# Kernel optimization log

Hardware: AMD Instinct MI355X
Metric: run time of the kernel (lower is better)

The kernel has to match this reference:

```python
import jax, jax.numpy as jnp
import numpy as np

HEADS = 8
DPH = 32  # n_features_per_head = 256 / 8
SCALE = 16.0  # sqrt(256)
EPS = 1e-5


def conv1x1(x, w, b):
    # x [B,C,H,W], w [O,C], b [O]
    return jnp.einsum('bchw,oc->bohw', x, w) + b[None, :, None, None]


def avg_pool2(x):
    # F.interpolate(scale_factor=0.5, bilinear, align_corners=False) with half-pixel
    # centers and integer-2 downsample is exactly 2x2 mean pooling.
    B, C, H, W = x.shape
    return x.reshape(B, C, H // 2, 2, W // 2, 2).mean(axis=(3, 5))


def grid_sample_bilinear(img, grid):
    # img [B,C,H,W], grid [B,Hg,Wg,2] (x,y) in [-1,1]; align_corners=False, zeros padding
    B, C, H, W = img.shape
    ix = (grid[..., 0] + 1.0) * (W * 0.5) - 0.5
    iy = (grid[..., 1] + 1.0) * (H * 0.5) - 0.5
    x0f = jnp.floor(ix); y0f = jnp.floor(iy)
    wx = ix - x0f; wy = iy - y0f
    x0 = x0f.astype(jnp.int32); y0 = y0f.astype(jnp.int32)
    flat = img.reshape(B, C, H * W)
    Hg, Wg = grid.shape[1], grid.shape[2]

    def gather(yy, xx):
        valid = ((xx >= 0) & (xx < W) & (yy >= 0) & (yy < H)).astype(img.dtype)
        idx = (jnp.clip(yy, 0, H - 1) * W + jnp.clip(xx, 0, W - 1)).reshape(B, 1, Hg * Wg)
        v = jnp.take_along_axis(flat, idx, axis=2).reshape(B, C, Hg, Wg)
        return v * valid[:, None]

    out = (gather(y0, x0) * ((1 - wy) * (1 - wx))[:, None]
           + gather(y0, x0 + 1) * ((1 - wy) * wx)[:, None]
           + gather(y0 + 1, x0) * (wy * (1 - wx))[:, None]
           + gather(y0 + 1, x0 + 1) * (wy * wx)[:, None])
    return out


def layernorm_channels(x, g, b):
    # LayerNormProxy(dim=1): normalize over channel axis per (b,h,w)
    mu = x.mean(axis=1, keepdims=True)
    var = ((x - mu) ** 2).mean(axis=1, keepdims=True)
    return (x - mu) / jnp.sqrt(var + EPS) * g[None, :, None, None] + b[None, :, None, None]


def setup_inputs() -> dict:
    key = jax.random.key(0)
    ks = jax.random.split(key, 16)
    B, D, H, W = 4, 256, 56, 56
    nH, nW = H // 2, W // 2
    s = 0.02
    inp = {
        'query': jax.random.normal(ks[0], (B, D, H, W), jnp.float32),
        'x': jax.random.normal(ks[1], (B, D, H, W), jnp.float32),
        'reference_points': jax.random.uniform(ks[2], (B * HEADS, nH, nW, 2), jnp.float32, -1.0, 1.0),
        'positional_embeddings': jax.random.normal(ks[3], (B, D, H, W), jnp.float32),
        'so_w1': jax.random.normal(ks[4], (D, 2 * D, 5, 5), jnp.float32) * s,
        'so_b1': jnp.zeros((D,), jnp.float32),
        'ln_g': jnp.ones((D,), jnp.float32),
        'ln_b': jnp.zeros((D,), jnp.float32),
        'so_w2': jax.random.normal(ks[5], (2 * HEADS, D), jnp.float32) * s,
        'so_b2': jax.random.normal(ks[6], (2 * HEADS,), jnp.float32),
        'q_w': jax.random.normal(ks[7], (D, D), jnp.float32) * s,
        'q_b': jnp.zeros((D,), jnp.float32),
        'k_w': jax.random.normal(ks[8], (DPH, DPH), jnp.float32) * s,
        'k_b': jnp.zeros((DPH,), jnp.float32),
        'v_w': jax.random.normal(ks[9], (DPH, DPH), jnp.float32) * s,
        'v_b': jnp.zeros((DPH,), jnp.float32),
        'o_w': jax.random.normal(ks[10], (D, D), jnp.float32) * s,
        'o_b': jnp.zeros((D,), jnp.float32),
    }
    return inp


def _forward(query, x, reference_points, positional_embeddings,
             so_w1, so_b1, ln_g, ln_b, so_w2, so_b2,
             q_w, q_b, k_w, k_b, v_w, v_b, o_w, o_b):
    B, D, H, W = query.shape
    # downsample + concat -> offset network
    rec = jnp.concatenate([avg_pool2(query), avg_pool2(x)], axis=1)  # [B,2D,nH,nW]
    h = jax.lax.conv_general_dilated(rec, so_w1, (1, 1), ((2, 2), (2, 2)),
                                     dimension_numbers=('NCHW', 'OIHW', 'NCHW'))
    h = h + so_b1[None, :, None, None]
    h = layernorm_channels(h, ln_g, ln_b)
    h = jax.nn.gelu(h, approximate=False)
    off = jnp.tanh(conv1x1(h, so_w2, so_b2))  # [B, 2*heads, nH, nW]
    nH, nW = off.shape[2], off.shape[3]
    # permute(0,2,3,1) -> view(B,nH,nW,heads,2) -> permute(0,3,1,2,4)
    off = off.transpose(0, 2, 3, 1).reshape(B, nH, nW, HEADS, 2)
    off = off.transpose(0, 3, 1, 2, 4).reshape(B * HEADS, nH, nW, 2)
    loc = jnp.clip(reference_points + off, -1.0, 1.0)
    sampled = grid_sample_bilinear(x.reshape(B * HEADS, DPH, H, W), loc)  # [B*h,dph,nH,nW]
    qe = query + positional_embeddings
    q = conv1x1(qe, q_w, q_b).reshape(B * HEADS, DPH, H * W)
    k = conv1x1(sampled, k_w, k_b).reshape(B * HEADS, DPH, nH * nW)
    v = conv1x1(sampled, v_w, v_b).reshape(B * HEADS, DPH, nH * nW)
    attn = jax.nn.softmax(jnp.einsum('bdq,bdk->bqk', q, k) / SCALE, axis=2)
    out = jnp.einsum('bqk,bdk->bdq', attn, v).reshape(B, D, H, W)
    return conv1x1(out, o_w, o_b)


def reference(query, x, reference_points, positional_embeddings,
              so_w1, so_b1, ln_g, ln_b, so_w2, so_b2,
              q_w, q_b, k_w, k_b, v_w, v_b, o_w, o_b):
    return _forward(query, x, reference_points, positional_embeddings,
                    so_w1, so_b1, ln_g, ln_b, so_w2, so_b2,
                    q_w, q_b, k_w, k_b, v_w, v_b, o_w, o_b)
```

## Files before the change

### kernel.cpp

```cpp
#include <hip/hip_runtime.h>
#include <hip/hip_bf16.h>

#define B_    4
#define D_    256
#define H_    56
#define W_    56
#define NH_   28
#define NW_   28
#define HEADS 8
#define DPH   32
#define NPOS  784
#define NS    3136
#define NSB   196

typedef unsigned short ushort_t;
typedef unsigned int uint_t;
typedef __attribute__((ext_vector_type(8))) short bf16x8;
typedef __attribute__((ext_vector_type(4))) float f32x4;

#define OFF_REC     0u
#define OFF_HPART   1605632u
#define OFF_WREPC   4816896u
#define OFF_LOC     8093696u
#define OFF_KTB     8946688u
#define OFF_VTB     9348096u
#define OFF_W256    9749568u
#define OFF_QPE     4816896u
#define OFF_QBF     0u
#define OFF_ATTNT   1605632u

__device__ __forceinline__ ushort_t bf16rne(float f) {
    uint_t u = __float_as_uint(f);
    return (ushort_t)((u + 0x7FFFu + ((u >> 16) & 1u)) >> 16);
}
__device__ __forceinline__ float ubf(ushort_t h) {
    return __uint_as_float(((uint_t)h) << 16);
}
__device__ __forceinline__ uint_t packsplit(float v) {
    ushort_t hi = bf16rne(v);
    ushort_t lo = bf16rne(v - ubf(hi));
    return ((uint_t)hi << 16) | (uint_t)lo;
}
__device__ __forceinline__ uint_t cvtpk_bf16(float a, float b) {
    uint_t r;
    asm("v_cvt_pk_bf16_f32 %0, %1, %2" : "=v"(r) : "v"(a), "v"(b));
    return r;
}
__device__ __forceinline__ bf16x8 mk8(uint_t a, uint_t b, uint_t c, uint_t d) {
    union { uint_t u[4]; bf16x8 v; } x;
    x.u[0] = a; x.u[1] = b; x.u[2] = c; x.u[3] = d;
    return x.v;
}

__global__ __launch_bounds__(256) void k_prep(const float* __restrict__ q,
                                              const float* __restrict__ x,
                                              const float* __restrict__ w1,
                                              const float* __restrict__ qw,
                                              const float* __restrict__ ow,
                                              uint_t* __restrict__ rec,
                                              ushort_t* __restrict__ wh,
                                              ushort_t* __restrict__ wl,
                                              ushort_t* __restrict__ w256) {
    const int bid = blockIdx.x;
    if (bid < 6272) {
        int idx = bid * 256 + threadIdx.x;
        int j = idx % NW_;
        int i = (idx / NW_) % NH_;
        int c = (idx / NPOS) % 512;
        int b = idx / (NPOS * 512);
        const float* src = (c < 256) ? q : x;
        int cc = (c < 256) ? c : (c - 256);
        const float* p = src + ((size_t)(b * 256 + cc) * H_ + i * 2) * W_ + j * 2;
        float v = 0.25f * (p[0] + p[1] + p[W_] + p[W_ + 1]);
        rec[idx] = packsplit(v);
    } else if (bid < 7872) {
        int idx = (bid - 6272) * 256 + threadIdx.x;
        int lane = idx & 63;
        int cbi  = (idx >> 6) & 15;
        int ocf  = (idx >> 10) & 15;
        int tap  = idx >> 14;
        int m_in = lane & 15, g = lane >> 4;
        int oc = ocf * 16 + m_in;
        int c0 = cbi * 32 + g * 8;
        const float* wp = w1 + ((size_t)oc * 512 + c0) * 25 + tap;
        uint_t hp[4], lp[4];
        #pragma unroll
        for (int j = 0; j < 4; ++j) {
            float v0 = wp[(size_t)(2 * j) * 25];
            float v1 = wp[(size_t)(2 * j + 1) * 25];
            ushort_t h0 = bf16rne(v0), h1 = bf16rne(v1);
            ushort_t l0 = bf16rne(v0 - ubf(h0)), l1 = bf16rne(v1 - ubf(h1));
            hp[j] = (uint_t)h0 | ((uint_t)h1 << 16);
            lp[j] = (uint_t)l0 | ((uint_t)l1 << 16);
        }
        *(uint4*)(wh + (size_t)idx * 8) = make_uint4(hp[0], hp[1], hp[2], hp[3]);
        *(uint4*)(wl + (size_t)idx * 8) = make_uint4(lp[0], lp[1], lp[2], lp[3]);
    } else {
        int idx = (bid - 7872) * 256 + threadIdx.x;
        int lane = idx & 63;
        int cbi  = (idx >> 6) & 7;
        int ocf  = idx >> 9;
        int n = lane & 15, g = lane >> 4;
        size_t src = (size_t)(ocf * 16 + n) * 256 + cbi * 32 + g * 8;
        uint_t qh[4], ql[4], oh[4], ol[4];
        #pragma unroll
        for (int j = 0; j < 4; ++j) {
            float q0 = qw[src + 2 * j], q1 = qw[src + 2 * j + 1];
            float o0 = ow[src + 2 * j], o1 = ow[src + 2 * j + 1];
            ushort_t qh0 = bf16rne(q0), qh1 = bf16rne(q1);
            ushort_t oh0 = bf16rne(o0), oh1 = bf16rne(o1);
            qh[j] = (uint_t)qh0 | ((uint_t)qh1 << 16);
            ql[j] = (uint_t)bf16rne(q0 - ubf(qh0)) | ((uint_t)bf16rne(q1 - ubf(qh1)) << 16);
            oh[j] = (uint_t)oh0 | ((uint_t)oh1 << 16);
            ol[j] = (uint_t)bf16rne(o0 - ubf(oh0)) | ((uint_t)bf16rne(o1 - ubf(oh1)) << 16);
        }
        size_t dst = (size_t)idx * 8;
        *(uint4*)(w256 + dst)          = make_uint4(qh[0], qh[1], qh[2], qh[3]);
        *(uint4*)(w256 + dst + 65536)  = make_uint4(ql[0], ql[1], ql[2], ql[3]);
        *(uint4*)(w256 + dst + 131072) = make_uint4(oh[0], oh[1], oh[2], oh[3]);
        *(uint4*)(w256 + dst + 196608) = make_uint4(ol[0], ol[1], ol[2], ol[3]);
    }
}

__global__ __launch_bounds__(512) void k_conv_mfma(const uint_t* __restrict__ rec,
                                                   const ushort_t* __restrict__ wrep_hi,
                                                   float* __restrict__ hpart) {
    const int bid = blockIdx.x;
    const int ntcs = bid & 7;
    const int u = bid >> 3;
    const int mt = u % 13;
    const int b  = u / 13;
    const int nt = ntcs & 1;
    const int cs = ntcs >> 1;

    const int tid  = threadIdx.x;
    const int lane = tid & 63;
    const int wid  = tid >> 6;
    const int wm = wid & 1, wn = wid >> 1;
    const int m_in = lane & 15, g = lane >> 4;

    const int p0  = mt * 64;
    const int ylo = p0 / 28;

    __shared__ __align__(16) ushort_t sA[16384];

    int plinb[2];
    #pragma unroll
    for (int mf = 0; mf < 2; ++mf) {
        int p = p0 + wm * 32 + mf * 16 + m_in;
        int y = p / 28, xx = p - y * 28;
        plinb[mf] = (y - ylo) * 32 + xx;
    }

    const int oc0 = nt * 128 + wn * 32;
    const int ocf0 = nt * 8 + wn * 2;
    const ushort_t* bp[2];
    #pragma unroll
    for (int nf = 0; nf < 2; ++nf)
        bp[nf] = wrep_hi + (size_t)(ocf0 + nf) * 8192 + (lane << 3);

    f32x4 acc[2][2];
    #pragma unroll
    for (int i = 0; i < 2; ++i)
        #pragma unroll
        for (int j = 0; j < 2; ++j)
            acc[i][j] = (f32x4){0.f, 0.f, 0.f, 0.f};

    int  s_pl[2], s_cg[2];
    bool s_ok[2];
    const uint_t* s_rp[2];
    #pragma unroll
    for (int it = 0; it < 2; ++it) {
        int v  = tid + it * 512;
        int cg = v & 3, pl = v >> 2;
        int ty = pl >> 5, tx = pl & 31;
        int yi = ylo - 2 + ty, xi = tx - 2;
        bool ok = (yi >= 0) && (yi < 28) && (xi >= 0) && (xi < 28);
        s_pl[it] = pl; s_cg[it] = cg; s_ok[it] = ok;
        int off = ok ? (yi * 28 + xi) : 0;
        s_rp[it] = rec + ((size_t)(b * 512 + cg * 8)) * NPOS + off;
    }
    uint_t st[2][8];

#define STAGE_LOAD(CB) do {                                                  \
    _Pragma("unroll")                                                        \
    for (int it_ = 0; it_ < 2; ++it_) {                                      \
        const uint_t* rp_ = s_rp[it_] + (size_t)(CB) * NPOS;                 \
        _Pragma("unroll")                                                    \
        for (int i_ = 0; i_ < 8; ++i_)                                       \
            st[it_][i_] = s_ok[it_] ? rp_[(size_t)i_ * NPOS] : 0u;           \
    } } while (0)

#define STAGE_WRITE() do {                                                   \
    _Pragma("unroll")                                                        \
    for (int it_ = 0; it_ < 2; ++it_) {                                      \
        uint_t hw_[4], lw_[4];                                               \
        _Pragma("unroll")                                                    \
        for (int j_ = 0; j_ < 4; ++j_) {                                     \
            hw_[j_] = (st[it_][2*j_] >> 16) | (st[it_][2*j_+1] & 0xFFFF0000u); \
            lw_[j_] = (st[it_][2*j_] & 0xFFFFu) | (st[it_][2*j_+1] << 16);   \
        }                                                                    \
        int pl_ = s_pl[it_];                                                 \
        int cw_ = s_cg[it_] ^ ((pl_ >> 1) & 3);                              \
        *(uint4*)(sA + pl_ * 32 + cw_ * 8) =                                 \
            make_uint4(hw_[0], hw_[1], hw_[2], hw_[3]);                      \
        *(uint4*)(sA + 8192 + pl_ * 32 + cw_ * 8) =                          \
            make_uint4(lw_[0], lw_[1], lw_[2], lw_[3]);                      \
    } } while (0)

#define LOADB(BH, BL, TAP, CBI) do {                                         \
    size_t tof_ = (size_t)(TAP) * 131072 + (size_t)(CBI) * 512;              \
    _Pragma("unroll")                                                        \
    for (int nf_ = 0; nf_ < 2; ++nf_) {                                      \
        BH[nf_] = *(const bf16x8*)(bp[nf_] + tof_);                          \
        BL[nf_] = *(const bf16x8*)(bp[nf_] + tof_ + 3276800u);               \
    } } while (0)

#define TAPBODY(BH, BL, TOFF) do {                                           \
    int to_ = (TOFF);                                                        \
    _Pragma("unroll")                                                        \
    for (int mf_ = 0; mf_ < 2; ++mf_) {                                      \
        const int pl_ = plinb[mf_] + to_;                                    \
        const int ao_ = (pl_ << 5) + ((g ^ ((pl_ >> 1) & 3)) << 3);          \
        bf16x8 ah_ = *(const bf16x8*)(sA + ao_);                             \
        bf16x8 al_ = *(const bf16x8*)(sA + 8192 + ao_);                      \
        _Pragma("unroll")                                                    \
        for (int nf_ = 0; nf_ < 2; ++nf_) {                                  \
            acc[mf_][nf_] = __builtin_amdgcn_mfma_f32_16x16x32_bf16(         \
                ah_, BH[nf_], acc[mf_][nf_], 0, 0, 0);                       \
            acc[mf_][nf_] = __builtin_amdgcn_mfma_f32_16x16x32_bf16(         \
                ah_, BL[nf_], acc[mf_][nf_], 0, 0, 0);                       \
            acc[mf_][nf_] = __builtin_amdgcn_mfma_f32_16x16x32_bf16(         \
                al_, BH[nf_], acc[mf_][nf_], 0, 0, 0);                       \
        } } } while (0)

    STAGE_LOAD(cs * 128);

    for (int ch = 0; ch < 4; ++ch) {
        const int cb  = cs * 128 + ch * 32;
        const int cbi = cs * 4 + ch;

        __syncthreads();
        STAGE_WRITE();
        __syncthreads();
        if (ch < 3) STAGE_LOAD(cb + 32);

        bf16x8 bh0[2], bl0[2], bh1[2], bl1[2];
        LOADB(bh0, bl0, 0, cbi);
        for (int t = 0; t < 24; t += 2) {
            int t1 = t + 1, t2 = (t + 2 <= 24) ? t + 2 : 24;
            LOADB(bh1, bl1, t1, cbi);
            TAPBODY(bh0, bl0, (t / 5) * 32 + (t % 5));
            LOADB(bh0, bl0, t2, cbi);
            TAPBODY(bh1, bl1, (t1 / 5) * 32 + (t1 % 5));
        }
        TAPBODY(bh0, bl0, 4 * 32 + 4);
    }

    #pragma unroll
    for (int mf = 0; mf < 2; ++mf) {
        int prow = p0 + wm * 32 + mf * 16 + g * 4;
        #pragma unroll
        for (int nf = 0; nf < 2; ++nf) {
            int oc = oc0 + nf * 16 + m_in;
            #pragma unroll
            for (int r = 0; r < 4; ++r) {
                int pos = prow + r;
                if (pos < NPOS)
                    hpart[(((size_t)(cs * 4 + b) * NPOS + pos) << 8) + oc] =
                        acc[mf][nf][r];
            }
        }
    }
#undef STAGE_LOAD
#undef STAGE_WRITE
#undef LOADB
#undef TAPBODY
}

__global__ __launch_bounds__(256) void k_lnoff(const float* __restrict__ hpart,
                                               const float* __restrict__ b1,
                                               const float* __restrict__ g,
                                               const float* __restrict__ bb,
                                               const float* __restrict__ w2,
                                               const float* __restrict__ b2,
                                               const float* __restrict__ ref,
                                               float* __restrict__ loc) {
    const int pos = blockIdx.x, b = blockIdx.y, c = threadIdx.x;
    float v = b1[c];
    #pragma unroll
    for (int cs = 0; cs < 4; ++cs)
        v += hpart[((size_t)((cs * 4 + b) * NPOS + pos)) * 256 + c];

    float s1 = v, s2 = v * v;
    #pragma unroll
    for (int m = 32; m >= 1; m >>= 1) {
        s1 += __shfl_xor(s1, m);
        s2 += __shfl_xor(s2, m);
    }
    __shared__ float r1[4], r2[4];
    const int wv = c >> 6, ln = c & 63;
    if (ln == 0) { r1[wv] = s1; r2[wv] = s2; }
    __syncthreads();
    s1 = r1[0] + r1[1] + r1[2] + r1[3];
    s2 = r2[0] + r2[1] + r2[2] + r2[3];
    const float mu  = s1 * (1.f / 256.f);
    const float var = s2 * (1.f / 256.f) - mu * mu;
    const float rstd = 1.f / sqrtf(var + 1e-5f);
    const float xn = (v - mu) * rstd * g[c] + bb[c];
    const float ge = 0.5f * xn * (1.f + erff(xn * 0.70710678118654752f));

    __shared__ float ro[4][16];
    for (int o = 0; o < 16; ++o) {
        float pv = ge * w2[o * 256 + c];
        #pragma unroll
        for (int m = 32; m >= 1; m >>= 1) pv += __shfl_xor(pv, m);
        if (ln == 0) ro[wv][o] = pv;
    }
    __syncthreads();
    if (c < 16) {
        float off = ro[0][c] + ro[1][c] + ro[2][c] + ro[3][c] + b2[c];
        float t = tanhf(off);
        int hd = c >> 1, comp = c & 1;
        size_t li = ((size_t)((b * 8 + hd) * NPOS + pos)) * 2 + comp;
        float l = ref[li] + t;
        loc[li] = fminf(1.f, fmaxf(-1.f, l));
    }
}

__global__ __launch_bounds__(64) void k_gskv(const float* __restrict__ x,
                                             const float* __restrict__ loc,
                                             const float* __restrict__ kw,
                                             const float* __restrict__ kb,
                                             const float* __restrict__ vw,
                                             const float* __restrict__ vb,
                                             ushort_t* __restrict__ ktb,
                                             ushort_t* __restrict__ vtb) {
    __shared__ __align__(16) float kl[1024], vl[1024];
    const int tid = threadIdx.x;
    for (int i = tid; i < 1024; i += 64) {
        int o = i >> 5, c = i & 31;
        kl[c * 32 + o] = kw[i];
        vl[c * 32 + o] = vw[i];
    }
    __syncthreads();

    int idx = blockIdx.x * 64 + tid;
    int pos = idx % NPOS;
    int bh  = idx / NPOS;
    float gx = loc[(size_t)idx * 2 + 0];
    float gy = loc[(size_t)idx * 2 + 1];
    float ix = (gx + 1.f) * 28.f - 0.5f;
    float iy = (gy + 1.f) * 28.f - 0.5f;
    float x0f = floorf(ix), y0f = floorf(iy);
    int x0 = (int)x0f, y0 = (int)y0f;
    float wx = ix - x0f, wy = iy - y0f;

    int xs[2] = { x0, x0 + 1 };
    int ys[2] = { y0, y0 + 1 };
    float wxs[2] = { 1.f - wx, wx };
    float wys[2] = { 1.f - wy, wy };
    int   cidx[4];
    float cw[4];
    #pragma unroll
    for (int a = 0; a < 2; ++a)
        #pragma unroll
        for (int bb2 = 0; bb2 < 2; ++bb2) {
            int yy = ys[a], xx = xs[bb2];
            bool inb = (xx >= 0) && (xx < W_) && (yy >= 0) && (yy < H_);
            int yyc = min(max(yy, 0), H_ - 1), xxc = min(max(xx, 0), W_ - 1);
            cidx[a * 2 + bb2] = yyc * W_ + xxc;
            cw[a * 2 + bb2] = inb ? (wys[a] * wxs[bb2]) : 0.f;
        }

    const float* xb = x + (size_t)bh * DPH * NS;
    float ak[32] = {}, av[32] = {};
    for (int c = 0; c < DPH; ++c) {
        const float* xc = xb + (size_t)c * NS;
        float sv = cw[0] * xc[cidx[0]] + cw[1] * xc[cidx[1]]
                 + cw[2] * xc[cidx[2]] + cw[3] * xc[cidx[3]];
        #pragma unroll
        for (int og = 0; og < 8; ++og) {
            float4 k4 = *(const float4*)&kl[c * 32 + og * 4];
            float4 v4 = *(const float4*)&vl[c * 32 + og * 4];
            ak[og * 4 + 0] = fmaf(sv, k4.x, ak[og * 4 + 0]);
            ak[og * 4 + 1] = fmaf(sv, k4.y, ak[og * 4 + 1]);
            ak[og * 4 + 2] = fmaf(sv, k4.z, ak[og * 4 + 2]);
            ak[og * 4 + 3] = fmaf(sv, k4.w, ak[og * 4 + 3]);
            av[og * 4 + 0] = fmaf(sv, v4.x, av[og * 4 + 0]);
            av[og * 4 + 1] = fmaf(sv, v4.y, av[og * 4 + 1]);
            av[og * 4 + 2] = fmaf(sv, v4.z, av[og * 4 + 2]);
            av[og * 4 + 3] = fmaf(sv, v4.w, av[og * 4 + 3]);
        }
    }
    uint_t kp[16];
    #pragma unroll
    for (int o = 0; o < 16; ++o)
        kp[o] = (uint_t)bf16rne(ak[2 * o] + kb[2 * o])
              | ((uint_t)bf16rne(ak[2 * o + 1] + kb[2 * o + 1]) << 16);
    uint4* kdst = (uint4*)(ktb + (size_t)idx * 32);
    kdst[0] = make_uint4(kp[0], kp[1], kp[2], kp[3]);
    kdst[1] = make_uint4(kp[4], kp[5], kp[6], kp[7]);
    kdst[2] = make_uint4(kp[8], kp[9], kp[10], kp[11]);
    kdst[3] = make_uint4(kp[12], kp[13], kp[14], kp[15]);
    #pragma unroll
    for (int o = 0; o < 32; ++o)
        vtb[((size_t)bh * 32 + o) * NPOS + pos] = bf16rne(av[o] + vb[o]);
}

__global__ __launch_bounds__(256) void k_qpe(const float* __restrict__ q,
                                             const float* __restrict__ pe,
                                             uint_t* __restrict__ qpe) {
    const int st = blockIdx.x, b = blockIdx.y;
    const int s0 = st * 64;
    __shared__ uint_t T[64 * 129];
    const int l = threadIdx.x & 63, w = threadIdx.x >> 6;

    for (int half = 0; half < 2; ++half) {
        #pragma unroll 4
        for (int cc = 0; cc < 32; ++cc) {
            int c = half * 128 + w * 32 + cc;
            size_t gi = (size_t)(b * 256 + c) * NS + s0 + l;
            T[l * 129 + w * 32 + cc] = packsplit(q[gi] + pe[gi]);
        }
        __syncthreads();
        #pragma unroll
        for (int it = 0; it < 4; ++it) {
            int u2 = threadIdx.x + it * 256;
            int sblk = u2 >> 8;
            int cbl  = (u2 >> 6) & 3;
            int lane = u2 & 63;
            int n = lane & 15, g = lane >> 4;
            const uint_t* src = T + (sblk * 16 + n) * 129 + cbl * 32 + g * 8;
            uint_t* dst = qpe + ((((size_t)b * NSB + st * 4 + sblk) * 8
                                  + half * 4 + cbl) * 64 + lane) * 8;
            *(uint4*)dst       = make_uint4(src[0], src[1], src[2], src[3]);
            *(uint4*)(dst + 4) = make_uint4(src[4], src[5], src[6], src[7]);
        }
        __syncthreads();
    }
}

template<int MODE>
__global__ __launch_bounds__(256) void k_proj(const uint_t* __restrict__ inT,
                                              const ushort_t* __restrict__ wh,
                                              const ushort_t* __restrict__ wl,
                                              const float* __restrict__ bias,
                                              float* __restrict__ outf,
                                              ushort_t* __restrict__ outb) {
    const int st = blockIdx.x, og = blockIdx.y, b = blockIdx.z;
    const int tid = threadIdx.x, lane = tid & 63, wid = tid >> 6;
    const int wsg = wid & 1, wo = wid >> 1;
    const int n = lane & 15, g = lane >> 4;
    const int s0 = st * 64 + wsg * 32;
    const int sb0 = s0 >> 4;
    const int oc0 = og * 64 + wo * 32;
    const int ocf0 = oc0 >> 4;

    f32x4 acc[2][2];
    #pragma unroll
    for (int i = 0; i < 2; ++i)
        #pragma unroll
        for (int j = 0; j < 2; ++j)
            acc[i][j] = (f32x4){0.f, 0.f, 0.f, 0.f};

    #pragma unroll 2
    for (int kf = 0; kf < 8; ++kf) {
        bf16x8 awh[2], awl[2];
        #pragma unroll
        for (int mf = 0; mf < 2; ++mf) {
            size_t a = (((size_t)(ocf0 + mf) * 8 + kf) * 64 + lane) * 8;
            awh[mf] = *(const bf16x8*)(wh + a);
            awl[mf] = *(const bf16x8*)(wl + a);
        }
        bf16x8 bh[2], bl[2];
        #pragma unroll
        for (int nf = 0; nf < 2; ++nf) {
            const uint_t* p = inT + ((((size_t)b * NSB + sb0 + nf) * 8 + kf) * 64 + lane) * 8;
            uint4 u = *(const uint4*)p, v = *(const uint4*)(p + 4);
            bh[nf] = mk8((u.x >> 16) | (u.y & 0xFFFF0000u),
                         (u.z >> 16) | (u.w & 0xFFFF0000u),
                         (v.x >> 16) | (v.y & 0xFFFF0000u),
                         (v.z >> 16) | (v.w & 0xFFFF0000u));
            bl[nf] = mk8((u.x & 0xFFFFu) | (u.y << 16),
                         (u.z & 0xFFFFu) | (u.w << 16),
                         (v.x & 0xFFFFu) | (v.y << 16),
                         (v.z & 0xFFFFu) | (v.w << 16));
        }
        #pragma unroll
        for (int mf = 0; mf < 2; ++mf)
            #pragma unroll
            for (int nf = 0; nf < 2; ++nf) {
                acc[mf][nf] = __builtin_amdgcn_mfma_f32_16x16x32_bf16(
                    awh[mf], bh[nf], acc[mf][nf], 0, 0, 0);
                acc[mf][nf] = __builtin_amdgcn_mfma_f32_16x16x32_bf16(
                    awh[mf], bl[nf], acc[mf][nf], 0, 0, 0);
                acc[mf][nf] = __builtin_amdgcn_mfma_f32_16x16x32_bf16(
                    awl[mf], bh[nf], acc[mf][nf], 0, 0, 0);
            }
    }

    #pragma unroll
    for (int mf = 0; mf < 2; ++mf) {
        const int ocr = oc0 + mf * 16 + g * 4;
        float bs[4];
        #pragma unroll
        for (int r = 0; r < 4; ++r) bs[r] = bias[ocr + r];
        #pragma unroll
        for (int nf = 0; nf < 2; ++nf) {
            if (MODE == 0) {
                const int cblk = oc0 >> 5;
                const int lane2 = (mf * 2 + (g >> 1)) * 16 + n;
                uint_t p0 = (uint_t)bf16rne(acc[mf][nf][0] + bs[0])
                          | ((uint_t)bf16rne(acc[mf][nf][1] + bs[1]) << 16);
                uint_t p1 = (uint_t)bf16rne(acc[mf][nf][2] + bs[2])
                          | ((uint_t)bf16rne(acc[mf][nf][3] + bs[3]) << 16);
                *(uint2*)(outb + (((size_t)b * NSB + sb0 + nf) * 8 + cblk) * 512
                          + lane2 * 8 + (g & 1) * 4) = make_uint2(p0, p1);
            } else {
                int sc = s0 + nf * 16 + n;
                #pragma unroll
                for (int r = 0; r < 4; ++r)
                    outf[(size_t)(b * 256 + ocr + r) * NS + sc] =
                        acc[mf][nf][r] + bs[r];
            }
        }
    }
}

__global__ __launch_bounds__(256) void k_attn_mfma(const ushort_t* __restrict__ qbf,
                                                   const ushort_t* __restrict__ ktb,
                                                   const ushort_t* __restrict__ vtb,
                                                   uint_t* __restrict__ attnT) {
    const int qt = blockIdx.x, bh = blockIdx.y;
    const int b = bh >> 3, head = bh & 7;
    const int tid = threadIdx.x, lane = tid & 63, wid = tid >> 6;
    const int n = lane & 15, g = lane >> 4;

    __shared__ __align__(16) ushort_t sP[4][32 * 72];

    const int q0 = qt * 128 + wid * 32;

    bf16x8 qf[2];
    #pragma unroll
    for (int nf = 0; nf < 2; ++nf) {
        int sb = min(q0 / 16 + nf, NSB - 1);
        qf[nf] = *(const bf16x8*)(qbf + ((((size_t)b * NSB + sb) * 8 + head) * 64 + lane) * 8);
    }

    const ushort_t* kbase = ktb + (size_t)bh * NPOS * 32;
    const ushort_t* vbase = vtb + (size_t)bh * 32 * NPOS;
    ushort_t* myP = sP[wid];

    f32x4 o_acc[2][2];
    #pragma unroll
    for (int i = 0; i < 2; ++i)
        #pragma unroll
        for (int j = 0; j < 2; ++j)
            o_acc[i][j] = (f32x4){0.f, 0.f, 0.f, 0.f};
    float mrun[2] = {-1e30f, -1e30f};
    float lrun[2] = {0.f, 0.f};

    for (int t = 0; t < 12; ++t) {
        const int kvt = t * 64;
        bf16x8 kf[4];
        #pragma unroll
        for (int mf = 0; mf < 4; ++mf)
            kf[mf] = *(const bf16x8*)(kbase + (size_t)(kvt + mf * 16 + n) * 32 + g * 8);
        bf16x8 vf[2][2];
        #pragma unroll
        for (int mv = 0; mv < 2; ++mv)
            #pragma unroll
            for (int kc = 0; kc < 2; ++kc)
                vf[mv][kc] = *(const bf16x8*)(vbase + (size_t)(mv * 16 + n) * NPOS
                                              + kvt + kc * 32 + g * 8);

        f32x4 acc[4][2];
        #pragma unroll
        for (int mf = 0; mf < 4; ++mf)
            #pragma unroll
            for (int nf = 0; nf < 2; ++nf)
                acc[mf][nf] = __builtin_amdgcn_mfma_f32_16x16x32_bf16(
                    kf[mf], qf[nf], (f32x4){0.f, 0.f, 0.f, 0.f}, 0, 0, 0);

        #pragma unroll
        for (int nf = 0; nf < 2; ++nf) {
            float s[4][4];
            float tmax = -1e30f;
            #pragma unroll
            for (int mf = 0; mf < 4; ++mf)
                #pragma unroll
                for (int r = 0; r < 4; ++r) {
                    s[mf][r] = acc[mf][nf][r] * (1.f / 16.f);
                    tmax = fmaxf(tmax, s[mf][r]);
                }
            tmax = fmaxf(tmax, __shfl_xor(tmax, 16));
            tmax = fmaxf(tmax, __shfl_xor(tmax, 32));
            float mnew = fmaxf(mrun[nf], tmax);
            float corr = __expf(mrun[nf] - mnew);
            mrun[nf] = mnew;
            float psum = 0.f;
            float p[4][4];
            #pragma unroll
            for (int mf = 0; mf < 4; ++mf)
                #pragma unroll
                for (int r = 0; r < 4; ++r) {
                    p[mf][r] = __expf(s[mf][r] - mnew);
                    psum += p[mf][r];
                }
            psum += __shfl_xor(psum, 16);
            psum += __shfl_xor(psum, 32);
            lrun[nf] = lrun[nf] * corr + psum;
            #pragma unroll
            for (int mv = 0; mv < 2; ++mv)
                #pragma unroll
                for (int r = 0; r < 4; ++r)
                    o_acc[mv][nf][r] *= corr;
            #pragma unroll
            for (int mf = 0; mf < 4; ++mf) {
                uint_t lo = cvtpk_bf16(p[mf][0], p[mf][1]);
                uint_t hi = cvtpk_bf16(p[mf][2], p[mf][3]);
                *(uint2*)(myP + (nf * 16 + n) * 72 + mf * 16 + g * 4) =
                    make_uint2(lo, hi);
            }
        }

        #pragma unroll
        for (int kc = 0; kc < 2; ++kc)
            #pragma unroll
            for (int nf = 0; nf < 2; ++nf) {
                bf16x8 pb = *(const bf16x8*)(myP + (nf * 16 + n) * 72
                                             + kc * 32 + g * 8);
                #pragma unroll
                for (int mv = 0; mv < 2; ++mv)
                    o_acc[mv][nf] = __builtin_amdgcn_mfma_f32_16x16x32_bf16(
                        vf[mv][kc], pb, o_acc[mv][nf], 0, 0, 0);
            }
    }

    {
        const int kvt = 768;
        bf16x8 kf0 = *(const bf16x8*)(kbase + (size_t)(kvt + n) * 32 + g * 8);
        bf16x8 vf[2];
        int kvo = kvt + g * 8; if (kvo > 776) kvo = 776;
        #pragma unroll
        for (int mv = 0; mv < 2; ++mv)
            vf[mv] = *(const bf16x8*)(vbase + (size_t)(mv * 16 + n) * NPOS + kvo);

        f32x4 acc0[2];
        #pragma unroll
        for (int nf = 0; nf < 2; ++nf)
            acc0[nf] = __builtin_amdgcn_mfma_f32_16x16x32_bf16(
                kf0, qf[nf], (f32x4){0.f, 0.f, 0.f, 0.f}, 0, 0, 0);

        #pragma unroll
        for (int nf = 0; nf < 2; ++nf) {
            float s[4], tmax = -1e30f;
            #pragma unroll
            for (int r = 0; r < 4; ++r) {
                s[r] = acc0[nf][r] * (1.f / 16.f);
                tmax = fmaxf(tmax, s[r]);
            }
            tmax = fmaxf(tmax, __shfl_xor(tmax, 16));
            tmax = fmaxf(tmax, __shfl_xor(tmax, 32));
            float mnew = fmaxf(mrun[nf], tmax);
            float corr = __expf(mrun[nf] - mnew);
            mrun[nf] = mnew;
            float psum = 0.f, p[4];
            #pragma unroll
            for (int r = 0; r < 4; ++r) { p[r] = __expf(s[r] - mnew); psum += p[r]; }
            psum += __shfl_xor(psum, 16);
            psum += __shfl_xor(psum, 32);
            lrun[nf] = lrun[nf] * corr + psum;
            #pragma unroll
            for (int mv = 0; mv < 2; ++mv)
                #pragma unroll
                for (int r = 0; r < 4; ++r)
                    o_acc[mv][nf][r] *= corr;
            uint_t lo = cvtpk_bf16(p[0], p[1]);
            uint_t hi = cvtpk_bf16(p[2], p[3]);
            *(uint2*)(myP + (nf * 16 + n) * 72 + g * 4) = make_uint2(lo, hi);
            *(uint2*)(myP + (nf * 16 + n) * 72 + 16 + g * 4) = make_uint2(0u, 0u);
        }
        #pragma unroll
        for (int nf = 0; nf < 2; ++nf) {
            bf16x8 pb = *(const bf16x8*)(myP + (nf * 16 + n) * 72 + g * 8);
            #pragma unroll
            for (int mv = 0; mv < 2; ++mv)
                o_acc[mv][nf] = __builtin_amdgcn_mfma_f32_16x16x32_bf16(
                    vf[mv], pb, o_acc[mv][nf], 0, 0, 0);
        }
    }

    #pragma unroll
    for (int nf = 0; nf < 2; ++nf) {
        if (q0 + nf * 16 < NS) {
            float inv = 1.f / lrun[nf];
            const size_t sbase = (((size_t)b * NSB + (q0 / 16 + nf)) * 8 + head) * 512;
            #pragma unroll
            for (int mv = 0; mv < 2; ++mv) {
                uint_t pk[4];
                #pragma unroll
                for (int r = 0; r < 4; ++r)
                    pk[r] = packsplit(o_acc[mv][nf][r] * inv);
                const int lane2 = (mv * 2 + (g >> 1)) * 16 + n;
                *(uint4*)(attnT + sbase + lane2 * 8 + (g & 1) * 4) =
                    make_uint4(pk[0], pk[1], pk[2], pk[3]);
            }
        }
    }
}

extern "C" void kernel_launch(void* const* d_in, const int* in_sizes, int n_in,
                              void* d_out, int out_size, void* d_ws, size_t ws_size,
                              hipStream_t stream) {
    const float* query = (const float*)d_in[0];
    const float* x     = (const float*)d_in[1];
    const float* refp  = (const float*)d_in[2];
    const float* pe    = (const float*)d_in[3];
    const float* w1    = (const float*)d_in[4];
    const float* b1    = (const float*)d_in[5];
    const float* lng   = (const float*)d_in[6];
    const float* lnb   = (const float*)d_in[7];
    const float* w2    = (const float*)d_in[8];
    const float* b2    = (const float*)d_in[9];
    const float* qw    = (const float*)d_in[10];
    const float* qb    = (const float*)d_in[11];
    const float* kw    = (const float*)d_in[12];
    const float* kb    = (const float*)d_in[13];
    const float* vw    = (const float*)d_in[14];
    const float* vb    = (const float*)d_in[15];
    const float* ow    = (const float*)d_in[16];
    const float* ob    = (const float*)d_in[17];

    float* ws  = (float*)d_ws;
    float* out = (float*)d_out;

    uint_t*   rec    = (uint_t*)(ws + OFF_REC);
    float*    hpart  = ws + OFF_HPART;
    float*    loc    = ws + OFF_LOC;
    ushort_t* ktb    = (ushort_t*)(ws + OFF_KTB);
    ushort_t* vtb    = (ushort_t*)(ws + OFF_VTB);
    ushort_t* w256   = (ushort_t*)(ws + OFF_W256);
    ushort_t* wrep_hi = (ushort_t*)(ws + OFF_WREPC);
    uint_t*   qpe    = (uint_t*)(ws + OFF_QPE);
    ushort_t* qbf    = (ushort_t*)(ws + OFF_QBF);
    uint_t*   attnT  = (uint_t*)(ws + OFF_ATTNT);

    ushort_t* qwh = w256;
    ushort_t* qwl = w256 + 65536;
    ushort_t* owh = w256 + 131072;
    ushort_t* owl = w256 + 196608;

    k_prep<<<7904, 256, 0, stream>>>(query, x, w1, qw, ow,
                                     rec, wrep_hi, wrep_hi + 3276800u, w256);
    k_conv_mfma<<<416, 512, 0, stream>>>(rec, wrep_hi, hpart);
    k_lnoff<<<dim3(784, 4), 256, 0, stream>>>(hpart, b1, lng, lnb, w2, b2, refp, loc);
    k_qpe<<<dim3(49, 4), 256, 0, stream>>>(query, pe, qpe);
    k_proj<0><<<dim3(49, 4, 4), 256, 0, stream>>>(qpe, qwh, qwl, qb, nullptr, qbf);
    k_gskv<<<392, 64, 0, stream>>>(x, loc, kw, kb, vw, vb, ktb, vtb);
    k_attn_mfma<<<dim3(25, 32), 256, 0, stream>>>(qbf, ktb, vtb, attnT);
    k_proj<1><<<dim3(49, 4, 4), 256, 0, stream>>>(attnT, owh, owl, ob, out, nullptr);
}
```

Before: 208.5 us.

## Store V in MFMA fragment-major layout so attention loads are contiguous

The gather/KV-projection kernel now stages each block's V output in shared memory and writes it out pre-swizzled in the exact per-lane bf16x8 fragment order the attention MFMA consumes, padded to 25 KV blocks of 32. The attention kernel then reads V fragments with fully coalesced 16-byte loads instead of strided row reads across NPOS. The grid changes to 13x32 blocks, so some threads are idle for padding, and the kernel gains an extra shared-memory pass and barrier.

```diff
diff --git a/kernel.cpp b/kernel.cpp
--- a/kernel.cpp
+++ b/kernel.cpp
@@ -12,6 +12,7 @@
 #define NPOS  784
 #define NS    3136
 #define NSB   196
+#define NKVB  25
 
 typedef unsigned short ushort_t;
 typedef unsigned int uint_t;
@@ -22,8 +23,8 @@
 #define OFF_HPART   1605632u
 #define OFF_WREPC   4816896u
 #define OFF_LOC     8093696u
+#define OFF_VFM     8143872u
 #define OFF_KTB     8946688u
-#define OFF_VTB     9348096u
 #define OFF_W256    9749568u
 #define OFF_QPE     4816896u
 #define OFF_QBF     0u
@@ -335,9 +336,11 @@
                                              const float* __restrict__ vw,
                                              const float* __restrict__ vb,
                                              ushort_t* __restrict__ ktb,
-                                             ushort_t* __restrict__ vtb) {
+                                             ushort_t* __restrict__ vfm) {
     __shared__ __align__(16) float kl[1024], vl[1024];
+    __shared__ __align__(16) ushort_t sV[32 * 66];
     const int tid = threadIdx.x;
+    const int bh = blockIdx.y;
     for (int i = tid; i < 1024; i += 64) {
         int o = i >> 5, c = i & 31;
         kl[c * 32 + o] = kw[i];
@@ -345,67 +348,86 @@
     }
     __syncthreads();
 
-    int idx = blockIdx.x * 64 + tid;
-    int pos = idx % NPOS;
-    int bh  = idx / NPOS;
-    float gx = loc[(size_t)idx * 2 + 0];
-    float gy = loc[(size_t)idx * 2 + 1];
-    float ix = (gx + 1.f) * 28.f - 0.5f;
-    float iy = (gy + 1.f) * 28.f - 0.5f;
-    float x0f = floorf(ix), y0f = floorf(iy);
-    int x0 = (int)x0f, y0 = (int)y0f;
-    float wx = ix - x0f, wy = iy - y0f;
-
-    int xs[2] = { x0, x0 + 1 };
-    int ys[2] = { y0, y0 + 1 };
-    float wxs[2] = { 1.f - wx, wx };
-    float wys[2] = { 1.f - wy, wy };
-    int   cidx[4];
-    float cw[4];
-    #pragma unroll
-    for (int a = 0; a < 2; ++a)
-        #pragma unroll
-        for (int bb2 = 0; bb2 < 2; ++bb2) {
-            int yy = ys[a], xx = xs[bb2];
-            bool inb = (xx >= 0) && (xx < W_) && (yy >= 0) && (yy < H_);
-            int yyc = min(max(yy, 0), H_ - 1), xxc = min(max(xx, 0), W_ - 1);
-            cidx[a * 2 + bb2] = yyc * W_ + xxc;
-            cw[a * 2 + bb2] = inb ? (wys[a] * wxs[bb2]) : 0.f;
-        }
-
-    const float* xb = x + (size_t)bh * DPH * NS;
+    const int pos = blockIdx.x * 64 + tid;
+    const bool valid = (pos < NPOS);
+    const int idx = bh * NPOS + (valid ? pos : 0);
+
     float ak[32] = {}, av[32] = {};
-    for (int c = 0; c < DPH; ++c) {
-        const float* xc = xb + (size_t)c * NS;
-        float sv = cw[0] * xc[cidx[0]] + cw[1] * xc[cidx[1]]
-                 + cw[2] * xc[cidx[2]] + cw[3] * xc[cidx[3]];
-        #pragma unroll
-        for (int og = 0; og < 8; ++og) {
-            float4 k4 = *(const float4*)&kl[c * 32 + og * 4];
-            float4 v4 = *(const float4*)&vl[c * 32 + og * 4];
-            ak[og * 4 + 0] = fmaf(sv, k4.x, ak[og * 4 + 0]);
-            ak[og * 4 + 1] = fmaf(sv, k4.y, ak[og * 4 + 1]);
-            ak[og * 4 + 2] = fmaf(sv, k4.z, ak[og * 4 + 2]);
-            ak[og * 4 + 3] = fmaf(sv, k4.w, ak[og * 4 + 3]);
-            av[og * 4 + 0] = fmaf(sv, v4.x, av[og * 4 + 0]);
-            av[og * 4 + 1] = fmaf(sv, v4.y, av[og * 4 + 1]);
-            av[og * 4 + 2] = fmaf(sv, v4.z, av[og * 4 + 2]);
-            av[og * 4 + 3] = fmaf(sv, v4.w, av[og * 4 + 3]);
-        }
-    }
-    uint_t kp[16];
-    #pragma unroll
-    for (int o = 0; o < 16; ++o)
-        kp[o] = (uint_t)bf16rne(ak[2 * o] + kb[2 * o])
-              | ((uint_t)bf16rne(ak[2 * o + 1] + kb[2 * o + 1]) << 16);
-    uint4* kdst = (uint4*)(ktb + (size_t)idx * 32);
-    kdst[0] = make_uint4(kp[0], kp[1], kp[2], kp[3]);
-    kdst[1] = make_uint4(kp[4], kp[5], kp[6], kp[7]);
-    kdst[2] = make_uint4(kp[8], kp[9], kp[10], kp[11]);
-    kdst[3] = make_uint4(kp[12], kp[13], kp[14], kp[15]);
+    if (valid) {
+        float gx = loc[(size_t)idx * 2 + 0];
+        float gy = loc[(size_t)idx * 2 + 1];
+        float ix = (gx + 1.f) * 28.f - 0.5f;
+        float iy = (gy + 1.f) * 28.f - 0.5f;
+        float x0f = floorf(ix), y0f = floorf(iy);
+        int x0 = (int)x0f, y0 = (int)y0f;
+        float wx = ix - x0f, wy = iy - y0f;
+
+        int xs[2] = { x0, x0 + 1 };
+        int ys[2] = { y0, y0 + 1 };
+        float wxs[2] = { 1.f - wx, wx };
+        float wys[2] = { 1.f - wy, wy };
+        int   cidx[4];
+        float cw[4];
+        #pragma unroll
+        for (int a = 0; a < 2; ++a)
+            #pragma unroll
+            for (int bb2 = 0; bb2 < 2; ++bb2) {
+                int yy = ys[a], xx = xs[bb2];
+                bool inb = (xx >= 0) && (xx < W_) && (yy >= 0) && (yy < H_);
+                int yyc = min(max(yy, 0), H_ - 1), xxc = min(max(xx, 0), W_ - 1);
+                cidx[a * 2 + bb2] = yyc * W_ + xxc;
+                cw[a * 2 + bb2] = inb ? (wys[a] * wxs[bb2]) : 0.f;
+            }
+
+        const float* xb = x + (size_t)bh * DPH * NS;
+        for (int c = 0; c < DPH; ++c) {
+            const float* xc = xb + (size_t)c * NS;
+            float sv = cw[0] * xc[cidx[0]] + cw[1] * xc[cidx[1]]
+                     + cw[2] * xc[cidx[2]] + cw[3] * xc[cidx[3]];
+            #pragma unroll
+            for (int og = 0; og < 8; ++og) {
+                float4 k4 = *(const float4*)&kl[c * 32 + og * 4];
+                float4 v4 = *(const float4*)&vl[c * 32 + og * 4];
+                ak[og * 4 + 0] = fmaf(sv, k4.x, ak[og * 4 + 0]);
+                ak[og * 4 + 1] = fmaf(sv, k4.y, ak[og * 4 + 1]);
+                ak[og * 4 + 2] = fmaf(sv, k4.z, ak[og * 4 + 2]);
+                ak[og * 4 + 3] = fmaf(sv, k4.w, ak[og * 4 + 3]);
+                av[og * 4 + 0] = fmaf(sv, v4.x, av[og * 4 + 0]);
+                av[og * 4 + 1] = fmaf(sv, v4.y, av[og * 4 + 1]);
+                av[og * 4 + 2] = fmaf(sv, v4.z, av[og * 4 + 2]);
+                av[og * 4 + 3] = fmaf(sv, v4.w, av[og * 4 + 3]);
+            }
+        }
+        uint_t kp[16];
+        #pragma unroll
+        for (int o = 0; o < 16; ++o)
+            kp[o] = (uint_t)bf16rne(ak[2 * o] + kb[2 * o])
+                  | ((uint_t)bf16rne(ak[2 * o + 1] + kb[2 * o + 1]) << 16);
+        uint4* kdst = (uint4*)(ktb + (size_t)idx * 32);
+        kdst[0] = make_uint4(kp[0], kp[1], kp[2], kp[3]);
+        kdst[1] = make_uint4(kp[4], kp[5], kp[6], kp[7]);
+        kdst[2] = make_uint4(kp[8], kp[9], kp[10], kp[11]);
+        kdst[3] = make_uint4(kp[12], kp[13], kp[14], kp[15]);
+    }
+
     #pragma unroll
     for (int o = 0; o < 32; ++o)
-        vtb[((size_t)bh * 32 + o) * NPOS + pos] = bf16rne(av[o] + vb[o]);
+        sV[o * 66 + tid] = valid ? bf16rne(av[o] + vb[o]) : (ushort_t)0;
+    __syncthreads();
+
+    #pragma unroll
+    for (int kvbl = 0; kvbl < 2; ++kvbl) {
+        int kvb = blockIdx.x * 2 + kvbl;
+        if (kvb < NKVB) {
+            int n = tid & 15, g = tid >> 4;
+            #pragma unroll
+            for (int dphf = 0; dphf < 2; ++dphf) {
+                const ushort_t* src = sV + (dphf * 16 + n) * 66 + kvbl * 32 + g * 8;
+                uint4 v = *(const uint4*)src;
+                *(uint4*)(vfm + ((((size_t)bh * NKVB + kvb) * 2 + dphf) * 64 + tid) * 8) = v;
+            }
+        }
+    }
 }
 
 __global__ __launch_bounds__(256) void k_qpe(const float* __restrict__ q,
@@ -530,7 +552,7 @@
 
 __global__ __launch_bounds__(256) void k_attn_mfma(const ushort_t* __restrict__ qbf,
                                                    const ushort_t* __restrict__ ktb,
-                                                   const ushort_t* __restrict__ vtb,
+                                                   const ushort_t* __restrict__ vfm,
                                                    uint_t* __restrict__ attnT) {
     const int qt = blockIdx.x, bh = blockIdx.y;
     const int b = bh >> 3, head = bh & 7;
@@ -549,7 +571,7 @@
     }
 
     const ushort_t* kbase = ktb + (size_t)bh * NPOS * 32;
-    const ushort_t* vbase = vtb + (size_t)bh * 32 * NPOS;
+    const ushort_t* vbase = vfm + (size_t)bh * NKVB * 1024;
     ushort_t* myP = sP[wid];
 
     f32x4 o_acc[2][2];
@@ -572,8 +594,8 @@
         for (int mv = 0; mv < 2; ++mv)
             #pragma unroll
             for (int kc = 0; kc < 2; ++kc)
-                vf[mv][kc] = *(const bf16x8*)(vbase + (size_t)(mv * 16 + n) * NPOS
-                                              + kvt + kc * 32 + g * 8);
+                vf[mv][kc] = *(const bf16x8*)(vbase
+                    + (((size_t)(t * 2 + kc) * 2 + mv) * 64 + lane) * 8);
 
         f32x4 acc[4][2];
         #pragma unroll
@@ -639,13 +661,11 @@
     }
 
     {
-        const int kvt = 768;
-        bf16x8 kf0 = *(const bf16x8*)(kbase + (size_t)(kvt + n) * 32 + g * 8);
+        bf16x8 kf0 = *(const bf16x8*)(kbase + (size_t)(768 + n) * 32 + g * 8);
         bf16x8 vf[2];
-        int kvo = kvt + g * 8; if (kvo > 776) kvo = 776;
         #pragma unroll
         for (int mv = 0; mv < 2; ++mv)
-            vf[mv] = *(const bf16x8*)(vbase + (size_t)(mv * 16 + n) * NPOS + kvo);
+            vf[mv] = *(const bf16x8*)(vbase + (((size_t)24 * 2 + mv) * 64 + lane) * 8);
 
         f32x4 acc0[2];
         #pragma unroll
@@ -740,7 +760,7 @@
     float*    hpart  = ws + OFF_HPART;
     float*    loc    = ws + OFF_LOC;
     ushort_t* ktb    = (ushort_t*)(ws + OFF_KTB);
-    ushort_t* vtb    = (ushort_t*)(ws + OFF_VTB);
+    ushort_t* vfm    = (ushort_t*)(ws + OFF_VFM);
     ushort_t* w256   = (ushort_t*)(ws + OFF_W256);
     ushort_t* wrep_hi = (ushort_t*)(ws + OFF_WREPC);
     uint_t*   qpe    = (uint_t*)(ws + OFF_QPE);
@@ -758,7 +778,7 @@
     k_lnoff<<<dim3(784, 4), 256, 0, stream>>>(hpart, b1, lng, lnb, w2, b2, refp, loc);
     k_qpe<<<dim3(49, 4), 256, 0, stream>>>(query, pe, qpe);
     k_proj<0><<<dim3(49, 4, 4), 256, 0, stream>>>(qpe, qwh, qwl, qb, nullptr, qbf);
-    k_gskv<<<392, 64, 0, stream>>>(x, loc, kw, kb, vw, vb, ktb, vtb);
-    k_attn_mfma<<<dim3(25, 32), 256, 0, stream>>>(qbf, ktb, vtb, attnT);
+    k_gskv<<<dim3(13, 32), 64, 0, stream>>>(x, loc, kw, kb, vw, vb, ktb, vfm);
+    k_attn_mfma<<<dim3(25, 32), 256, 0, stream>>>(qbf, ktb, vfm, attnT);
     k_proj<1><<<dim3(49, 4, 4), 256, 0, stream>>>(attnT, owh, owl, ob, out, nullptr);
 }
```

After: 204.4 us (median of 2 runs). No clear change (-1.9%).
